# Optimization experiments

Hardware: AMD Instinct MI355X
Metric: run time of the kernel (lower is better)

The kernel has to match this reference:

```python
import jax, jax.numpy as jnp
import numpy as np

B, C, CI, H, W = 4, 256, 128, 64, 64  # batch, in_channels, inter_channels, spatial


def conv1x1(x, w, b):
    # x: [B,C,H,W], w: [O,C], b: [O] -> [B,O,H,W]
    return jnp.einsum('bchw,oc->bohw', x, w) + b[None, :, None, None]


def setup_inputs() -> dict:
    key = jax.random.key(0)
    ks = jax.random.split(key, 9)
    s = 0.02
    return {
        'x':  jax.random.normal(ks[0], (B, C, H, W), dtype=jnp.float32),
        'Wg': jax.random.normal(ks[1], (CI, C), dtype=jnp.float32) * s,
        'bg': jnp.zeros((CI,), dtype=jnp.float32),
        'Wt': jax.random.normal(ks[2], (CI, C), dtype=jnp.float32) * s,
        'bt': jnp.zeros((CI,), dtype=jnp.float32),
        'Wp': jax.random.normal(ks[3], (CI, C), dtype=jnp.float32) * s,
        'bp': jnp.zeros((CI,), dtype=jnp.float32),
        'Wo': jax.random.normal(ks[4], (C, CI), dtype=jnp.float32) * s,
        'bo': jnp.zeros((C,), dtype=jnp.float32),
    }


def reference(x, Wg, bg, Wt, bt, Wp, bp, Wo, bo):
    b, c, h, w = x.shape
    n = h * w
    g  = conv1x1(x, Wg, bg).reshape(b, -1, n)   # [B,CI,N]
    th = conv1x1(x, Wt, bt).reshape(b, -1, n)   # [B,CI,N]
    ph = conv1x1(x, Wp, bp).reshape(b, -1, n)   # [B,CI,N]
    f = jnp.einsum('bci,bcj->bij', th, ph)      # [B,N,N] unscaled scores
    a = jax.nn.softmax(f, axis=-1)
    y = jnp.einsum('bij,bcj->bci', a, g)        # [B,CI,N]
    y = y.reshape(b, -1, h, w)
    return conv1x1(y, Wo, bo) + x
```

## Files before the change

kernel.cpp:

```cpp
#include <hip/hip_runtime.h>
#include <math.h>

#define B_  4
#define C_  256
#define CI_ 128
#define N_  4096

typedef short s16x8  __attribute__((ext_vector_type(8)));
typedef float f32x4  __attribute__((ext_vector_type(4)));
typedef float f32x16 __attribute__((ext_vector_type(16)));

__device__ inline ushort f2bf(float f) {
    unsigned int u = __float_as_uint(f);
    u += 0x7FFF + ((u >> 16) & 1);
    return (ushort)(u >> 16);
}
__device__ inline float bf2f(ushort u) {
    return __uint_as_float(((unsigned int)u) << 16);
}

__device__ inline unsigned pkbf(float a, float b) {
    unsigned r;
    asm("v_cvt_pk_bf16_f32 %0, %1, %2" : "=v"(r) : "v"(a), "v"(b));
    return r;
}
__device__ inline void plswap(unsigned &x, unsigned &y) {
    asm volatile("v_permlane32_swap_b32 %0, %1" : "+v"(x), "+v"(y));
}

__device__ inline void gload_lds16(const void* g, void* l) {
    __builtin_amdgcn_global_load_lds(
        (const __attribute__((address_space(1))) unsigned int*)g,
        (__attribute__((address_space(3))) unsigned int*)l, 16, 0, 0);
}

__device__ inline void block_sync_lds() {
    asm volatile("s_waitcnt lgkmcnt(0)" ::: "memory");
    __builtin_amdgcn_s_barrier();
    asm volatile("" ::: "memory");
}

__global__ __launch_bounds__(256) void wcast_kernel(
    const float* __restrict__ Wg, const float* __restrict__ Wt,
    const float* __restrict__ Wp, const float* __restrict__ Wo,
    const float* __restrict__ bg, const float* __restrict__ bt,
    const float* __restrict__ bp,
    ushort* __restrict__ Wcat, ushort* __restrict__ Wobf,
    float* __restrict__ bcat)
{
    int i = blockIdx.x * 256 + threadIdx.x;
    if (i < 32768)       Wcat[i] = f2bf(Wg[i]);
    else if (i < 65536)  Wcat[i] = f2bf(Wt[i - 32768]);
    else if (i < 98304)  Wcat[i] = f2bf(Wp[i - 65536]);
    else if (i < 131072) Wobf[i - 98304] = f2bf(Wo[i - 98304]);
    if (i < 128)         bcat[i] = bg[i];
    else if (i < 256)    bcat[i] = bt[i - 128];
    else if (i < 384)    bcat[i] = bp[i - 256];
}

__global__ __launch_bounds__(256) void xt_kernel(
    const float* __restrict__ x, ushort* __restrict__ xT)
{
    __shared__ ushort Ls[64][72];
    const int b = blockIdx.z, c0 = blockIdx.y * 64, n0 = blockIdx.x * 64;
    const float* xb = x + ((size_t)b * C_ + c0) * N_ + n0;
    const int t = threadIdx.x;
    #pragma unroll
    for (int r = 0; r < 4; r++) {
        int idx = t + 256 * r;
        int c = idx >> 4, n4 = (idx & 15) * 4;
        float4 v = *(const float4*)&xb[(size_t)c * N_ + n4];
        ushort4 o;
        o.x = f2bf(v.x); o.y = f2bf(v.y); o.z = f2bf(v.z); o.w = f2bf(v.w);
        *(ushort4*)&Ls[c][n4] = o;
    }
    __syncthreads();
    ushort* xTb = xT + ((size_t)b * N_ + n0) * C_ + c0;
    #pragma unroll
    for (int r = 0; r < 2; r++) {
        int idx = t + 256 * r;
        int n = idx >> 3, c8 = (idx & 7) * 8;
        ushort tmp[8];
        #pragma unroll
        for (int u = 0; u < 8; u++) tmp[u] = Ls[c8 + u][n];
        *(uint4*)&xTb[(size_t)n * C_ + c8] = *(uint4*)tmp;
    }
}

__global__ __launch_bounds__(256) void proj_kernel(
    const ushort* __restrict__ Wcat, const float* __restrict__ bcat,
    const ushort* __restrict__ xT,
    ushort* __restrict__ g, ushort* __restrict__ tht, ushort* __restrict__ pht)
{
    __shared__ ushort Ws[64][72];
    __shared__ ushort Xs[64][72];
    const int b = blockIdx.z, mt = blockIdx.y, n0 = blockIdx.x * 64;
    const int t = threadIdx.x, wv = t >> 6, lane = t & 63;
    const int g4 = lane >> 4, ln = lane & 15;
    const ushort* Wsrc = Wcat + (size_t)mt * 64 * C_;
    const ushort* Xsrc = xT + ((size_t)b * N_ + n0) * C_;

    f32x4 acc[4];
    #pragma unroll
    for (int i = 0; i < 4; i++) acc[i] = (f32x4){0.f, 0.f, 0.f, 0.f};

    for (int k0 = 0; k0 < C_; k0 += 64) {
        block_sync_lds();
        #pragma unroll
        for (int r = 0; r < 2; r++) {
            int idx = t + 256 * r;
            int row = idx >> 3, k8 = (idx & 7) * 8;
            *(uint4*)&Ws[row][k8] = *(const uint4*)&Wsrc[(size_t)row * C_ + k0 + k8];
            *(uint4*)&Xs[row][k8] = *(const uint4*)&Xsrc[(size_t)row * C_ + k0 + k8];
        }
        block_sync_lds();
        if (mt < 2) {
            #pragma unroll
            for (int kk = 0; kk < 2; kk++) {
                s16x8 aW = *(const s16x8*)&Ws[16 * wv + ln][32 * kk + 8 * g4];
                #pragma unroll
                for (int nt = 0; nt < 4; nt++) {
                    s16x8 bX = *(const s16x8*)&Xs[16 * nt + ln][32 * kk + 8 * g4];
                    acc[nt] = __builtin_amdgcn_mfma_f32_16x16x32_bf16(aW, bX, acc[nt], 0, 0, 0);
                }
            }
        } else {
            #pragma unroll
            for (int kk = 0; kk < 2; kk++) {
                s16x8 aX = *(const s16x8*)&Xs[16 * wv + ln][32 * kk + 8 * g4];
                #pragma unroll
                for (int ct = 0; ct < 4; ct++) {
                    s16x8 bW = *(const s16x8*)&Ws[16 * ct + ln][32 * kk + 8 * g4];
                    acc[ct] = __builtin_amdgcn_mfma_f32_16x16x32_bf16(aX, bW, acc[ct], 0, 0, 0);
                }
            }
        }
    }

    if (mt < 2) {
        ushort* ob = g + (size_t)b * CI_ * N_;
        #pragma unroll
        for (int r = 0; r < 4; r++) {
            int mloc = 16 * wv + 4 * g4 + r;
            float bi = bcat[mt * 64 + mloc];
            #pragma unroll
            for (int nt = 0; nt < 4; nt++)
                ob[(size_t)(mt * 64 + mloc) * N_ + n0 + 16 * nt + ln] = f2bf(acc[nt][r] + bi);
        }
    } else {
        ushort* ob = ((mt < 4) ? tht : pht) + (size_t)b * N_ * CI_;
        int cib = ((mt - 2) & 1) * 64;
        #pragma unroll
        for (int r = 0; r < 4; r++) {
            int nloc = 16 * wv + 4 * g4 + r;
            #pragma unroll
            for (int ct = 0; ct < 4; ct++) {
                float bi = bcat[mt * 64 + 16 * ct + ln];
                ob[(size_t)(n0 + nloc) * CI_ + cib + 16 * ct + ln] = f2bf(acc[ct][r] + bi);
            }
        }
    }
}


__device__ inline float build_pa(const f32x16& S, s16x8& f0, s16x8& f1) {
    unsigned w[8];
    #pragma unroll
    for (int e = 0; e < 8; e++)
        w[e] = pkbf(__expf(S[2 * e]), __expf(S[2 * e + 1]));
    float ls = 0.f;
    #pragma unroll
    for (int e = 0; e < 8; e++)
        ls += __uint_as_float(w[e] << 16) + __uint_as_float(w[e] & 0xFFFF0000u);
    plswap(w[0], w[2]);
    plswap(w[1], w[3]);
    plswap(w[4], w[6]);
    plswap(w[5], w[7]);
    union { unsigned u[4]; s16x8 v; } A, B;
    A.u[0] = w[0]; A.u[1] = w[1]; A.u[2] = w[2]; A.u[3] = w[3];
    B.u[0] = w[4]; B.u[1] = w[5]; B.u[2] = w[6]; B.u[3] = w[7];
    f0 = A.v; f1 = B.v;
    return ls;
}

template <int NC>
__global__ __launch_bounds__(256, 3) void attn_mfma_kernel(
    const ushort* __restrict__ qn,
    const ushort* __restrict__ kn,
    const ushort* __restrict__ vm,
    ushort* __restrict__ Opart,
    float* __restrict__ lbuf)
{
    constexpr int JC = N_ / NC;
    __shared__ __align__(16) char smemB[32768];
    char* KsB = smemB;
    char* VtB = smemB + 16384;

    constexpr int NI = N_ / 128;
    constexpr int nb = NI * NC * B_;
    int flat = (blockIdx.z * NC + blockIdx.y) * NI + blockIdx.x;
    int nf   = (flat & 7) * (nb / 8) + (flat >> 3);
    const int i0    = (nf % NI) * 128;
    const int chunk = (nf / NI) % NC;
    const int b     = nf / (NI * NC);
    const int jbase = chunk * JC;

    const int t    = threadIdx.x;
    const int wv   = t >> 6;
    const int lane = t & 63;
    const int n32  = lane & 31;
    const int h    = lane >> 5;
    const int swz  = (n32 & 7) << 4;

    const ushort* qb = qn + ((size_t)b * N_ + i0) * CI_;
    const char* kB = (const char*)(kn + (size_t)b * N_ * CI_);
    const char* vB = (const char*)(vm + (size_t)b * CI_ * N_);

    s16x8 aQ[8];
    #pragma unroll
    for (int kk = 0; kk < 8; kk++)
        aQ[kk] = *(const s16x8*)(qb + (size_t)(32 * wv + n32) * CI_ + 16 * kk + 8 * h);

    f32x16 Oacc[4];
    #pragma unroll
    for (int dt = 0; dt < 4; dt++)
        #pragma unroll
        for (int e = 0; e < 16; e++) Oacc[dt][e] = 0.f;
    float lsum = 0.f;

    const int kr = lane >> 4;
    const int kc = (lane & 15) << 4;
    const int vr = lane >> 3;
    const int vc = (lane & 7) << 4;

    for (int jt = jbase; jt < jbase + JC; jt += 64) {
        block_sync_lds();

        #pragma unroll
        for (int r = 0; r < 4; r++) {
            int c   = (wv << 2) + r;
            int row = (c << 2) + kr;
            int src = ((jt + row) << 8) + (kc ^ ((row & 7) << 4));
            gload_lds16(kB + src, KsB + (c << 10));
        }
        #pragma unroll
        for (int r = 0; r < 4; r++) {
            int c   = (wv << 2) + r;
            int row = (c << 3) + vr;
            int src = row * (N_ * 2) + (jt << 1) + (vc ^ ((row & 7) << 4));
            gload_lds16(vB + src, VtB + (c << 10));
        }
        asm volatile("s_waitcnt vmcnt(0)" ::: "memory");
        __builtin_amdgcn_s_barrier();

        s16x8 pa[4];
        f32x16 S0;
        #pragma unroll
        for (int e = 0; e < 16; e++) S0[e] = 0.f;
        __builtin_amdgcn_s_setprio(1);
        #pragma unroll
        for (int kk = 0; kk < 8; kk++) {
            s16x8 aK0 = *(const s16x8*)(KsB + (n32 << 8) + (((kk << 5) + (h << 4)) ^ swz));
            S0 = __builtin_amdgcn_mfma_f32_32x32x16_bf16(aK0, aQ[kk], S0, 0, 0, 0);
        }
        __builtin_amdgcn_s_setprio(0);
        lsum += build_pa(S0, pa[0], pa[1]);

        f32x16 S1;
        #pragma unroll
        for (int e = 0; e < 16; e++) S1[e] = 0.f;
        __builtin_amdgcn_s_setprio(1);
        #pragma unroll
        for (int kk = 0; kk < 8; kk++) {
            s16x8 aK1 = *(const s16x8*)(KsB + 8192 + (n32 << 8) + (((kk << 5) + (h << 4)) ^ swz));
            S1 = __builtin_amdgcn_mfma_f32_32x32x16_bf16(aK1, aQ[kk], S1, 0, 0, 0);
        }
        __builtin_amdgcn_s_setprio(0);
        lsum += build_pa(S1, pa[2], pa[3]);

        __builtin_amdgcn_s_setprio(1);
        #pragma unroll
        for (int dt = 0; dt < 4; dt++) {
            #pragma unroll
            for (int kk = 0; kk < 4; kk++) {
                s16x8 bV = *(const s16x8*)(VtB + ((32 * dt + n32) << 7)
                                               + (((kk << 5) + (h << 4)) ^ swz));
                Oacc[dt] = __builtin_amdgcn_mfma_f32_32x32x16_bf16(pa[kk], bV, Oacc[dt], 0, 0, 0);
            }
        }
        __builtin_amdgcn_s_setprio(0);
    }

    ushort* Ob = Opart + (size_t)chunk * (B_ * N_ * CI_) + ((size_t)b * N_ + i0) * CI_;
    #pragma unroll
    for (int rg = 0; rg < 16; rg++) {
        int R = (rg & 3) + 8 * (rg >> 2) + 4 * h;
        int q = 32 * wv + R;
        #pragma unroll
        for (int dt = 0; dt < 4; dt++)
            Ob[(size_t)q * CI_ + 32 * dt + n32] = f2bf(Oacc[dt][rg]);
    }
    float ot  = __shfl_xor(lsum, 32);
    float tot = lsum + ot;
    if (h == 0)
        lbuf[((size_t)chunk * B_ + b) * N_ + i0 + 32 * wv + n32] = tot;
}

template <int NC>
__global__ __launch_bounds__(256) void outgemm_kernel(
    const ushort* __restrict__ Wobf, const float* __restrict__ bo,
    const ushort* __restrict__ Opart, const float* __restrict__ lbuf,
    const float* __restrict__ x, float* __restrict__ out)
{
    __shared__ ushort Ws[64][72];
    __shared__ ushort Ys[64][72];
    const int b = blockIdx.z, m0 = blockIdx.y * 64, n0 = blockIdx.x * 64;
    const int t = threadIdx.x, wv = t >> 6, lane = t & 63;
    const int g4 = lane >> 4, ln = lane & 15;
    const ushort* Wsrc = Wobf + (size_t)m0 * CI_;
    const size_t cs = (size_t)B_ * N_ * CI_;

    f32x4 acc[4];
    #pragma unroll
    for (int i = 0; i < 4; i++) acc[i] = (f32x4){0.f, 0.f, 0.f, 0.f};

    for (int k0 = 0; k0 < CI_; k0 += 64) {
        block_sync_lds();
        #pragma unroll
        for (int r = 0; r < 2; r++) {
            int idx = t + 256 * r;
            int row = idx >> 3, k8 = (idx & 7) * 8;
            *(uint4*)&Ws[row][k8] = *(const uint4*)&Wsrc[(size_t)row * CI_ + k0 + k8];
            size_t obase = ((size_t)b * N_ + n0 + row) * CI_ + k0 + k8;
            float lsum = 0.f;
            #pragma unroll
            for (int c = 0; c < NC; c++)
                lsum += lbuf[((size_t)c * B_ + b) * N_ + n0 + row];
            float inv = 1.0f / lsum;
            float osum[8];
            #pragma unroll
            for (int u = 0; u < 8; u++) osum[u] = 0.f;
            #pragma unroll
            for (int c = 0; c < NC; c++) {
                ushort oc[8];
                *(uint4*)oc = *(const uint4*)&Opart[(size_t)c * cs + obase];
                #pragma unroll
                for (int u = 0; u < 8; u++) osum[u] += bf2f(oc[u]);
            }
            ushort yo[8];
            #pragma unroll
            for (int u = 0; u < 8; u++) yo[u] = f2bf(osum[u] * inv);
            *(uint4*)&Ys[row][k8] = *(uint4*)yo;
        }
        block_sync_lds();
        #pragma unroll
        for (int kk = 0; kk < 2; kk++) {
            s16x8 aW = *(const s16x8*)&Ws[16 * wv + ln][32 * kk + 8 * g4];
            #pragma unroll
            for (int nt = 0; nt < 4; nt++) {
                s16x8 bY = *(const s16x8*)&Ys[16 * nt + ln][32 * kk + 8 * g4];
                acc[nt] = __builtin_amdgcn_mfma_f32_16x16x32_bf16(aW, bY, acc[nt], 0, 0, 0);
            }
        }
    }

    float* outb = out + (size_t)b * C_ * N_;
    const float* xb = x + (size_t)b * C_ * N_;
    #pragma unroll
    for (int r = 0; r < 4; r++) {
        int m = m0 + 16 * wv + 4 * g4 + r;
        float bi = bo[m];
        #pragma unroll
        for (int nt = 0; nt < 4; nt++) {
            size_t idx = (size_t)m * N_ + n0 + 16 * nt + ln;
            outb[idx] = acc[nt][r] + bi + xb[idx];
        }
    }
}

extern "C" void kernel_launch(void* const* d_in, const int* in_sizes, int n_in,
                              void* d_out, int out_size, void* d_ws, size_t ws_size,
                              hipStream_t stream) {
    const float* x  = (const float*)d_in[0];
    const float* Wg = (const float*)d_in[1];
    const float* bg = (const float*)d_in[2];
    const float* Wt = (const float*)d_in[3];
    const float* bt = (const float*)d_in[4];
    const float* Wp = (const float*)d_in[5];
    const float* bp = (const float*)d_in[6];
    const float* Wo = (const float*)d_in[7];
    const float* bo = (const float*)d_in[8];
    float* out = (float*)d_out;

    const bool big = ws_size >= 46925312ull;
    const int NC = big ? 8 : 4;

    char* w = (char*)d_ws;
    size_t opart_sz = (size_t)NC * B_ * N_ * CI_ * sizeof(ushort);
    ushort* xT    = (ushort*)w;
    ushort* Opart = (ushort*)w;
    ushort* g     = (ushort*)(w + opart_sz);
    ushort* tht   = (ushort*)(w + opart_sz + 4194304);
    ushort* pht   = (ushort*)(w + opart_sz + 8388608);
    ushort* Wcat  = (ushort*)(w + opart_sz + 12582912);
    ushort* Wobf  = (ushort*)(w + opart_sz + 12582912 + 196608);
    float*  bcat  = (float*) (w + opart_sz + 12582912 + 262144);
    float*  lbuf  = (float*) (w + opart_sz + 12582912 + 263680);

    dim3 blk(256);
    wcast_kernel<<<512, blk, 0, stream>>>(Wg, Wt, Wp, Wo, bg, bt, bp, Wcat, Wobf, bcat);
    xt_kernel<<<dim3(N_ / 64, C_ / 64, B_), blk, 0, stream>>>(x, xT);
    proj_kernel<<<dim3(N_ / 64, 6, B_), blk, 0, stream>>>(Wcat, bcat, xT, g, tht, pht);
    if (big) {
        attn_mfma_kernel<8><<<dim3(N_ / 128, 8, B_), blk, 0, stream>>>(tht, pht, g, Opart, lbuf);
        outgemm_kernel<8><<<dim3(N_ / 64, C_ / 64, B_), blk, 0, stream>>>(Wobf, bo, Opart, lbuf, x, out);
    } else {
        attn_mfma_kernel<4><<<dim3(N_ / 128, 4, B_), blk, 0, stream>>>(tht, pht, g, Opart, lbuf);
        outgemm_kernel<4><<<dim3(N_ / 64, C_ / 64, B_), blk, 0, stream>>>(Wobf, bo, Opart, lbuf, x, out);
    }
}
```

Before: 156.2 us.

## Double-buffer attention K/V tiles, fuse prep kernels, merge projection blocks

```diff
diff --git a/kernel.cpp b/kernel.cpp
--- a/kernel.cpp
+++ b/kernel.cpp
@@ -40,31 +40,34 @@
     asm volatile("" ::: "memory");
 }
 
-__global__ __launch_bounds__(256) void wcast_kernel(
+__global__ __launch_bounds__(256) void prep_kernel(
     const float* __restrict__ Wg, const float* __restrict__ Wt,
     const float* __restrict__ Wp, const float* __restrict__ Wo,
     const float* __restrict__ bg, const float* __restrict__ bt,
     const float* __restrict__ bp,
     ushort* __restrict__ Wcat, ushort* __restrict__ Wobf,
-    float* __restrict__ bcat)
-{
-    int i = blockIdx.x * 256 + threadIdx.x;
-    if (i < 32768)       Wcat[i] = f2bf(Wg[i]);
-    else if (i < 65536)  Wcat[i] = f2bf(Wt[i - 32768]);
-    else if (i < 98304)  Wcat[i] = f2bf(Wp[i - 65536]);
-    else if (i < 131072) Wobf[i - 98304] = f2bf(Wo[i - 98304]);
-    if (i < 128)         bcat[i] = bg[i];
-    else if (i < 256)    bcat[i] = bt[i - 128];
-    else if (i < 384)    bcat[i] = bp[i - 256];
-}
-
-__global__ __launch_bounds__(256) void xt_kernel(
+    float* __restrict__ bcat,
     const float* __restrict__ x, ushort* __restrict__ xT)
 {
     __shared__ ushort Ls[64][72];
-    const int b = blockIdx.z, c0 = blockIdx.y * 64, n0 = blockIdx.x * 64;
+    const int bid = blockIdx.x;
+    const int t = threadIdx.x;
+    if (bid < 512) {
+        int i = bid * 256 + t;
+        if (i < 32768)       Wcat[i] = f2bf(Wg[i]);
+        else if (i < 65536)  Wcat[i] = f2bf(Wt[i - 32768]);
+        else if (i < 98304)  Wcat[i] = f2bf(Wp[i - 65536]);
+        else if (i < 131072) Wobf[i - 98304] = f2bf(Wo[i - 98304]);
+        if (i < 128)         bcat[i] = bg[i];
+        else if (i < 256)    bcat[i] = bt[i - 128];
+        else if (i < 384)    bcat[i] = bp[i - 256];
+        return;
+    }
+    int idx2 = bid - 512;
+    const int n0 = (idx2 & 63) * 64;
+    const int c0 = ((idx2 >> 6) & 3) * 64;
+    const int b  = idx2 >> 8;
     const float* xb = x + ((size_t)b * C_ + c0) * N_ + n0;
-    const int t = threadIdx.x;
     #pragma unroll
     for (int r = 0; r < 4; r++) {
         int idx = t + 256 * r;
@@ -92,71 +95,80 @@
     const ushort* __restrict__ xT,
     ushort* __restrict__ g, ushort* __restrict__ tht, ushort* __restrict__ pht)
 {
-    __shared__ ushort Ws[64][72];
+    __shared__ ushort Ws[192][72];
     __shared__ ushort Xs[64][72];
-    const int b = blockIdx.z, mt = blockIdx.y, n0 = blockIdx.x * 64;
+    const int b = blockIdx.z, yy = blockIdx.y, n0 = blockIdx.x * 64;
     const int t = threadIdx.x, wv = t >> 6, lane = t & 63;
     const int g4 = lane >> 4, ln = lane & 15;
-    const ushort* Wsrc = Wcat + (size_t)mt * 64 * C_;
     const ushort* Xsrc = xT + ((size_t)b * N_ + n0) * C_;
 
-    f32x4 acc[4];
-    #pragma unroll
-    for (int i = 0; i < 4; i++) acc[i] = (f32x4){0.f, 0.f, 0.f, 0.f};
+    f32x4 accg[4], acct[2][4];
+    #pragma unroll
+    for (int i = 0; i < 4; i++) {
+        accg[i] = (f32x4){0.f, 0.f, 0.f, 0.f};
+        acct[0][i] = (f32x4){0.f, 0.f, 0.f, 0.f};
+        acct[1][i] = (f32x4){0.f, 0.f, 0.f, 0.f};
+    }
 
     for (int k0 = 0; k0 < C_; k0 += 64) {
         block_sync_lds();
+        #pragma unroll
+        for (int r = 0; r < 6; r++) {
+            int idx = t + 256 * r;
+            int row = idx >> 3, k8 = (idx & 7) * 8;
+            int srow = ((row >> 6) * 2 + yy) * 64 + (row & 63);
+            *(uint4*)&Ws[row][k8] = *(const uint4*)&Wcat[(size_t)srow * C_ + k0 + k8];
+        }
         #pragma unroll
         for (int r = 0; r < 2; r++) {
             int idx = t + 256 * r;
             int row = idx >> 3, k8 = (idx & 7) * 8;
-            *(uint4*)&Ws[row][k8] = *(const uint4*)&Wsrc[(size_t)row * C_ + k0 + k8];
             *(uint4*)&Xs[row][k8] = *(const uint4*)&Xsrc[(size_t)row * C_ + k0 + k8];
         }
         block_sync_lds();
-        if (mt < 2) {
-            #pragma unroll
-            for (int kk = 0; kk < 2; kk++) {
-                s16x8 aW = *(const s16x8*)&Ws[16 * wv + ln][32 * kk + 8 * g4];
-                #pragma unroll
-                for (int nt = 0; nt < 4; nt++) {
-                    s16x8 bX = *(const s16x8*)&Xs[16 * nt + ln][32 * kk + 8 * g4];
-                    acc[nt] = __builtin_amdgcn_mfma_f32_16x16x32_bf16(aW, bX, acc[nt], 0, 0, 0);
-                }
-            }
-        } else {
-            #pragma unroll
-            for (int kk = 0; kk < 2; kk++) {
-                s16x8 aX = *(const s16x8*)&Xs[16 * wv + ln][32 * kk + 8 * g4];
+        #pragma unroll
+        for (int kk = 0; kk < 2; kk++) {
+            s16x8 aW = *(const s16x8*)&Ws[16 * wv + ln][32 * kk + 8 * g4];
+            #pragma unroll
+            for (int nt = 0; nt < 4; nt++) {
+                s16x8 bX = *(const s16x8*)&Xs[16 * nt + ln][32 * kk + 8 * g4];
+                accg[nt] = __builtin_amdgcn_mfma_f32_16x16x32_bf16(aW, bX, accg[nt], 0, 0, 0);
+            }
+            s16x8 aX = *(const s16x8*)&Xs[16 * wv + ln][32 * kk + 8 * g4];
+            #pragma unroll
+            for (int mi = 0; mi < 2; mi++) {
                 #pragma unroll
                 for (int ct = 0; ct < 4; ct++) {
-                    s16x8 bW = *(const s16x8*)&Ws[16 * ct + ln][32 * kk + 8 * g4];
-                    acc[ct] = __builtin_amdgcn_mfma_f32_16x16x32_bf16(aX, bW, acc[ct], 0, 0, 0);
+                    s16x8 bW = *(const s16x8*)&Ws[64 + 64 * mi + 16 * ct + ln][32 * kk + 8 * g4];
+                    acct[mi][ct] = __builtin_amdgcn_mfma_f32_16x16x32_bf16(aX, bW, acct[mi][ct], 0, 0, 0);
                 }
             }
         }
     }
 
-    if (mt < 2) {
+    {
         ushort* ob = g + (size_t)b * CI_ * N_;
         #pragma unroll
         for (int r = 0; r < 4; r++) {
             int mloc = 16 * wv + 4 * g4 + r;
-            float bi = bcat[mt * 64 + mloc];
+            float bi = bcat[yy * 64 + mloc];
             #pragma unroll
             for (int nt = 0; nt < 4; nt++)
-                ob[(size_t)(mt * 64 + mloc) * N_ + n0 + 16 * nt + ln] = f2bf(acc[nt][r] + bi);
-        }
-    } else {
-        ushort* ob = ((mt < 4) ? tht : pht) + (size_t)b * N_ * CI_;
-        int cib = ((mt - 2) & 1) * 64;
+                ob[(size_t)(yy * 64 + mloc) * N_ + n0 + 16 * nt + ln] = f2bf(accg[nt][r] + bi);
+        }
+    }
+    #pragma unroll
+    for (int mi = 0; mi < 2; mi++) {
+        int mt = 2 + 2 * mi + yy;
+        ushort* ob = (mi == 0 ? tht : pht) + (size_t)b * N_ * CI_;
+        int cib = yy * 64;
         #pragma unroll
         for (int r = 0; r < 4; r++) {
             int nloc = 16 * wv + 4 * g4 + r;
             #pragma unroll
             for (int ct = 0; ct < 4; ct++) {
                 float bi = bcat[mt * 64 + 16 * ct + ln];
-                ob[(size_t)(n0 + nloc) * CI_ + cib + 16 * ct + ln] = f2bf(acc[ct][r] + bi);
+                ob[(size_t)(n0 + nloc) * CI_ + cib + 16 * ct + ln] = f2bf(acct[mi][ct][r] + bi);
             }
         }
     }
@@ -183,27 +195,43 @@
     return ls;
 }
 
-template <int NC>
-__global__ __launch_bounds__(256, 3) void attn_mfma_kernel(
+#define STAGE_KV(bufofs, jsrc) do {                                          \
+    _Pragma("unroll")                                                        \
+    for (int r_ = 0; r_ < 4; r_++) {                                         \
+        int c_   = (wv << 2) + r_;                                           \
+        int row_ = (c_ << 2) + kr;                                           \
+        int src_ = (((jsrc) + row_) << 8) + (kc ^ ((row_ & 7) << 4));        \
+        gload_lds16(kB + src_, smemB + (bufofs) + (c_ << 10));               \
+    }                                                                        \
+    _Pragma("unroll")                                                        \
+    for (int r_ = 0; r_ < 4; r_++) {                                         \
+        int c_   = (wv << 2) + r_;                                           \
+        int row_ = (c_ << 3) + vr;                                           \
+        int src_ = row_ * (N_ * 2) + ((jsrc) << 1) + (vc ^ ((row_ & 7) << 4));\
+        gload_lds16(vB + src_, smemB + (bufofs) + 16384 + (c_ << 10));       \
+    }                                                                        \
+} while (0)
+
+#define NC_ 4
+#define JC_ (N_ / NC_)
+
+__global__ __launch_bounds__(256, 2) void attn_mfma_kernel(
     const ushort* __restrict__ qn,
     const ushort* __restrict__ kn,
     const ushort* __restrict__ vm,
     ushort* __restrict__ Opart,
     float* __restrict__ lbuf)
 {
-    constexpr int JC = N_ / NC;
-    __shared__ __align__(16) char smemB[32768];
-    char* KsB = smemB;
-    char* VtB = smemB + 16384;
+    __shared__ __align__(16) char smemB[65536];
 
     constexpr int NI = N_ / 128;
-    constexpr int nb = NI * NC * B_;
-    int flat = (blockIdx.z * NC + blockIdx.y) * NI + blockIdx.x;
+    constexpr int nb = NI * NC_ * B_;
+    int flat = (blockIdx.z * NC_ + blockIdx.y) * NI + blockIdx.x;
     int nf   = (flat & 7) * (nb / 8) + (flat >> 3);
     const int i0    = (nf % NI) * 128;
-    const int chunk = (nf / NI) % NC;
-    const int b     = nf / (NI * NC);
-    const int jbase = chunk * JC;
+    const int chunk = (nf / NI) % NC_;
+    const int b     = nf / (NI * NC_);
+    const int jbase = chunk * JC_;
 
     const int t    = threadIdx.x;
     const int wv   = t >> 6;
@@ -212,10 +240,10 @@
     const int h    = lane >> 5;
     const int swz  = (n32 & 7) << 4;
 
-    const ushort* qb = qn + ((size_t)b * N_ + i0) * CI_;
     const char* kB = (const char*)(kn + (size_t)b * N_ * CI_);
     const char* vB = (const char*)(vm + (size_t)b * CI_ * N_);
 
+    const ushort* qb = qn + ((size_t)b * N_ + i0) * CI_;
     s16x8 aQ[8];
     #pragma unroll
     for (int kk = 0; kk < 8; kk++)
@@ -233,62 +261,63 @@
     const int vr = lane >> 3;
     const int vc = (lane & 7) << 4;
 
-    for (int jt = jbase; jt < jbase + JC; jt += 64) {
+    STAGE_KV(0, jbase);
+    int buf = 0;
+    for (int jt = jbase; jt < jbase + JC_; jt += 64) {
+        if (jt + 64 < jbase + JC_) {
+            STAGE_KV(buf ^ 32768, jt + 64);
+            asm volatile("s_waitcnt vmcnt(8)" ::: "memory");
+        } else {
+            asm volatile("s_waitcnt vmcnt(0)" ::: "memory");
+        }
+        __builtin_amdgcn_s_barrier();
+        asm volatile("" ::: "memory");
+
+        const char* Kc = smemB + buf;
+        const char* Vc = smemB + buf + 16384;
+
+        s16x8 pa[4];
+        {
+            f32x16 S0;
+            #pragma unroll
+            for (int e = 0; e < 16; e++) S0[e] = 0.f;
+            __builtin_amdgcn_s_setprio(1);
+            #pragma unroll
+            for (int kk = 0; kk < 8; kk++) {
+                s16x8 aK = *(const s16x8*)(Kc + (n32 << 8) + (((kk << 5) + (h << 4)) ^ swz));
+                S0 = __builtin_amdgcn_mfma_f32_32x32x16_bf16(aK, aQ[kk], S0, 0, 0, 0);
+            }
+            __builtin_amdgcn_s_setprio(0);
+            lsum += build_pa(S0, pa[0], pa[1]);
+        }
+        {
+            f32x16 S1;
+            #pragma unroll
+            for (int e = 0; e < 16; e++) S1[e] = 0.f;
+            __builtin_amdgcn_s_setprio(1);
+            #pragma unroll
+            for (int kk = 0; kk < 8; kk++) {
+                s16x8 aK = *(const s16x8*)(Kc + 8192 + (n32 << 8) + (((kk << 5) + (h << 4)) ^ swz));
+                S1 = __builtin_amdgcn_mfma_f32_32x32x16_bf16(aK, aQ[kk], S1, 0, 0, 0);
+            }
+            __builtin_amdgcn_s_setprio(0);
+            lsum += build_pa(S1, pa[2], pa[3]);
+        }
+
+        __builtin_amdgcn_s_setprio(1);
+        #pragma unroll
+        for (int dt = 0; dt < 4; dt++) {
+            #pragma unroll
+            for (int kk = 0; kk < 4; kk++) {
+                s16x8 bV = *(const s16x8*)(Vc + ((32 * dt + n32) << 7)
+                                              + (((kk << 5) + (h << 4)) ^ swz));
+                Oacc[dt] = __builtin_amdgcn_mfma_f32_32x32x16_bf16(pa[kk], bV, Oacc[dt], 0, 0, 0);
+            }
+        }
+        __builtin_amdgcn_s_setprio(0);
+
         block_sync_lds();
-
-        #pragma unroll
-        for (int r = 0; r < 4; r++) {
-            int c   = (wv << 2) + r;
-            int row = (c << 2) + kr;
-            int src = ((jt + row) << 8) + (kc ^ ((row & 7) << 4));
-            gload_lds16(kB + src, KsB + (c << 10));
-        }
-        #pragma unroll
-        for (int r = 0; r < 4; r++) {
-            int c   = (wv << 2) + r;
-            int row = (c << 3) + vr;
-            int src = row * (N_ * 2) + (jt << 1) + (vc ^ ((row & 7) << 4));
-            gload_lds16(vB + src, VtB + (c << 10));
-        }
-        asm volatile("s_waitcnt vmcnt(0)" ::: "memory");
-        __builtin_amdgcn_s_barrier();
-
-        s16x8 pa[4];
-        f32x16 S0;
-        #pragma unroll
-        for (int e = 0; e < 16; e++) S0[e] = 0.f;
-        __builtin_amdgcn_s_setprio(1);
-        #pragma unroll
-        for (int kk = 0; kk < 8; kk++) {
-            s16x8 aK0 = *(const s16x8*)(KsB + (n32 << 8) + (((kk << 5) + (h << 4)) ^ swz));
-            S0 = __builtin_amdgcn_mfma_f32_32x32x16_bf16(aK0, aQ[kk], S0, 0, 0, 0);
-        }
-        __builtin_amdgcn_s_setprio(0);
-        lsum += build_pa(S0, pa[0], pa[1]);
-
-        f32x16 S1;
-        #pragma unroll
-        for (int e = 0; e < 16; e++) S1[e] = 0.f;
-        __builtin_amdgcn_s_setprio(1);
-        #pragma unroll
-        for (int kk = 0; kk < 8; kk++) {
-            s16x8 aK1 = *(const s16x8*)(KsB + 8192 + (n32 << 8) + (((kk << 5) + (h << 4)) ^ swz));
-            S1 = __builtin_amdgcn_mfma_f32_32x32x16_bf16(aK1, aQ[kk], S1, 0, 0, 0);
-        }
-        __builtin_amdgcn_s_setprio(0);
-        lsum += build_pa(S1, pa[2], pa[3]);
-
-        __builtin_amdgcn_s_setprio(1);
-        #pragma unroll
-        for (int dt = 0; dt < 4; dt++) {
-            #pragma unroll
-            for (int kk = 0; kk < 4; kk++) {
-                s16x8 bV = *(const s16x8*)(VtB + ((32 * dt + n32) << 7)
-                                               + (((kk << 5) + (h << 4)) ^ swz));
-                Oacc[dt] = __builtin_amdgcn_mfma_f32_32x32x16_bf16(pa[kk], bV, Oacc[dt], 0, 0, 0);
-            }
-        }
-        __builtin_amdgcn_s_setprio(0);
+        buf ^= 32768;
     }
 
     ushort* Ob = Opart + (size_t)chunk * (B_ * N_ * CI_) + ((size_t)b * N_ + i0) * CI_;
@@ -306,7 +335,6 @@
         lbuf[((size_t)chunk * B_ + b) * N_ + i0 + 32 * wv + n32] = tot;
 }
 
-template <int NC>
 __global__ __launch_bounds__(256) void outgemm_kernel(
     const ushort* __restrict__ Wobf, const float* __restrict__ bo,
     const ushort* __restrict__ Opart, const float* __restrict__ lbuf,
@@ -334,14 +362,14 @@
             size_t obase = ((size_t)b * N_ + n0 + row) * CI_ + k0 + k8;
             float lsum = 0.f;
             #pragma unroll
-            for (int c = 0; c < NC; c++)
+            for (int c = 0; c < NC_; c++)
                 lsum += lbuf[((size_t)c * B_ + b) * N_ + n0 + row];
             float inv = 1.0f / lsum;
             float osum[8];
             #pragma unroll
             for (int u = 0; u < 8; u++) osum[u] = 0.f;
             #pragma unroll
-            for (int c = 0; c < NC; c++) {
+            for (int c = 0; c < NC_; c++) {
                 ushort oc[8];
                 *(uint4*)oc = *(const uint4*)&Opart[(size_t)c * cs + obase];
                 #pragma unroll
@@ -392,30 +420,21 @@
     const float* bo = (const float*)d_in[8];
     float* out = (float*)d_out;
 
-    const bool big = ws_size >= 46925312ull;
-    const int NC = big ? 8 : 4;
-
     char* w = (char*)d_ws;
-    size_t opart_sz = (size_t)NC * B_ * N_ * CI_ * sizeof(ushort);
     ushort* xT    = (ushort*)w;
     ushort* Opart = (ushort*)w;
-    ushort* g     = (ushort*)(w + opart_sz);
-    ushort* tht   = (ushort*)(w + opart_sz + 4194304);
-    ushort* pht   = (ushort*)(w + opart_sz + 8388608);
-    ushort* Wcat  = (ushort*)(w + opart_sz + 12582912);
-    ushort* Wobf  = (ushort*)(w + opart_sz + 12582912 + 196608);
-    float*  bcat  = (float*) (w + opart_sz + 12582912 + 262144);
-    float*  lbuf  = (float*) (w + opart_sz + 12582912 + 263680);
+    ushort* g     = (ushort*)(w + 16777216);
+    ushort* tht   = (ushort*)(w + 20971520);
+    ushort* pht   = (ushort*)(w + 25165824);
+    ushort* Wcat  = (ushort*)(w + 29360128);
+    ushort* Wobf  = (ushort*)(w + 29556736);
+    float*  bcat  = (float*) (w + 29622272);
+    float*  lbuf  = (float*) (w + 29623808);
 
     dim3 blk(256);
-    wcast_kernel<<<512, blk, 0, stream>>>(Wg, Wt, Wp, Wo, bg, bt, bp, Wcat, Wobf, bcat);
-    xt_kernel<<<dim3(N_ / 64, C_ / 64, B_), blk, 0, stream>>>(x, xT);
-    proj_kernel<<<dim3(N_ / 64, 6, B_), blk, 0, stream>>>(Wcat, bcat, xT, g, tht, pht);
-    if (big) {
-        attn_mfma_kernel<8><<<dim3(N_ / 128, 8, B_), blk, 0, stream>>>(tht, pht, g, Opart, lbuf);
-        outgemm_kernel<8><<<dim3(N_ / 64, C_ / 64, B_), blk, 0, stream>>>(Wobf, bo, Opart, lbuf, x, out);
-    } else {
-        attn_mfma_kernel<4><<<dim3(N_ / 128, 4, B_), blk, 0, stream>>>(tht, pht, g, Opart, lbuf);
-        outgemm_kernel<4><<<dim3(N_ / 64, C_ / 64, B_), blk, 0, stream>>>(Wobf, bo, Opart, lbuf, x, out);
-    }
-}
+    prep_kernel<<<1536, blk, 0, stream>>>(Wg, Wt, Wp, Wo, bg, bt, bp,
+                                          Wcat, Wobf, bcat, x, xT);
+    proj_kernel<<<dim3(N_ / 64, 2, B_), blk, 0, stream>>>(Wcat, bcat, xT, g, tht, pht);
+    attn_mfma_kernel<<<dim3(N_ / 128, NC_, B_), blk, 0, stream>>>(tht, pht, g, Opart, lbuf);
+    outgemm_kernel<<<dim3(N_ / 64, C_ / 64, B_), blk, 0, stream>>>(Wobf, bo, Opart, lbuf, x, out);
+}
```

Result: faster. 150.9 us (-3.4%).
